# Kernel tuning notes

Measured on AMD Instinct MI355X. Metric: run time of the kernel, lower is better.

The kernel has to match this reference:

```python
import jax, jax.numpy as jnp
import numpy as np
from jax import lax

N_CLASS, SOS, EOS, NEG = 5, 0, 4, -10000.0


def _lstm_dir(x, Wih, Whh, bih, bhh, reverse):
    # x: (T, B, Din); PyTorch gate order i, f, g, o
    T, B, _ = x.shape
    Hd = Whh.shape[1]
    h0 = jnp.zeros((B, Hd), x.dtype)

    def step(carry, xt):
        h, c = carry
        g = xt @ Wih.T + h @ Whh.T + bih + bhh
        i, f, gg, o = jnp.split(g, 4, axis=-1)
        c = jax.nn.sigmoid(f) * c + jax.nn.sigmoid(i) * jnp.tanh(gg)
        h = jax.nn.sigmoid(o) * jnp.tanh(c)
        return (h, c), h

    xs = x[::-1] if reverse else x
    _, hs = lax.scan(step, (h0, h0), xs)
    return hs[::-1] if reverse else hs


def _forward(input_ids, tags, mask, emb, convs, lstm_params, lin_w, lin_b, transition):
    T, B = mask.shape
    x = emb[input_ids][:, None]  # (N, 1, L, E)
    pooled = []
    for w, b in convs:  # w: (K, 1, size, E)
        c = lax.conv_general_dilated(x, w, (1, 1), 'VALID',
                                     dimension_numbers=('NCHW', 'OIHW', 'NCHW'))
        c = jax.nn.relu(c[..., 0] + b[None, :, None])  # (N, K, L-size+1)
        pooled.append(jnp.max(c, axis=2))              # max-pool over length
    para = jnp.concatenate(pooled, axis=1)             # (N, 3K)
    h = para.reshape(B, T, -1).transpose(1, 0, 2)      # (T, B, 3K); equal para_len
    for (Wf, Uf, bf, cf, Wb, Ub, bb, cb) in lstm_params:  # 2-layer BiLSTM (eval: no dropout)
        hf = _lstm_dir(h, Wf, Uf, bf, cf, False)
        hb = _lstm_dir(h, Wb, Ub, bb, cb, True)
        h = jnp.concatenate([hf, hb], axis=-1)
    m = mask[..., None]
    feats = ((h * m) @ lin_w.T + lin_b) * m            # (T, B, 5)

    # CRF forward algorithm (log partition)
    alpha0 = jnp.full((B, N_CLASS), NEG, feats.dtype).at[:, SOS].set(0.0)

    def step(alpha, inp):
        feat, mt = inp
        s = alpha[:, None, :] + transition[None] + feat[:, :, None]
        new = jax.nn.logsumexp(s, axis=-1)
        return new * mt[:, None] + alpha * (1.0 - mt[:, None]), None

    alpha, _ = lax.scan(step, alpha0, (feats, mask))
    fwd_score = jax.nn.logsumexp(alpha + transition[EOS][None], axis=-1)

    # gold path score
    tags_ext = jnp.concatenate([jnp.full((1, B), SOS, tags.dtype), tags], 0)  # (T+1, B)
    emit = jnp.take_along_axis(feats, tags[..., None], axis=-1)[..., 0]       # (T, B)
    trans = transition[tags_ext[1:], tags_ext[:-1]]                           # (T, B)
    gold = jnp.sum((emit + trans) * mask, axis=0)
    lengths = mask.sum(0).astype(jnp.int32)
    last = tags_ext[lengths, jnp.arange(B)]
    gold = gold + transition[EOS, last]
    return (fwd_score - gold).sum()


def setup_inputs() -> dict:
    key = jax.random.key(0)
    ks = jax.random.split(key, 32)
    B, T, L, V, E, K, H = 8, 64, 64, 50000, 768, 256, 64
    N = B * T
    inp = {}
    inp['input_ids'] = jax.random.randint(ks[0], (N, L), 1, V)
    inp['tags'] = jax.random.randint(ks[1], (T, B), 1, 4)  # B/I/O tags
    inp['mask'] = jnp.ones((T, B), jnp.float32)
    inp['para_len'] = jnp.full((B,), T, jnp.int32)
    inp['emb'] = jax.random.normal(ks[2], (V, E)) * 0.1
    for i, sz in enumerate((3, 4, 5)):
        inp[f'cw{sz}'] = jax.random.normal(ks[3 + i], (K, 1, sz, E)) * (1.0 / np.sqrt(sz * E))
        inp[f'cb{sz}'] = jnp.zeros((K,), jnp.float32)
    kidx = 6
    for layer, din in ((0, 3 * K), (1, 2 * H)):
        for d in 'fb':
            inp[f'Wih{layer}{d}'] = jax.random.normal(ks[kidx], (4 * H, din)) * (1.0 / np.sqrt(din)); kidx += 1
            inp[f'Whh{layer}{d}'] = jax.random.normal(ks[kidx], (4 * H, H)) * (1.0 / np.sqrt(H)); kidx += 1
            inp[f'bih{layer}{d}'] = jnp.zeros((4 * H,), jnp.float32)
            inp[f'bhh{layer}{d}'] = jnp.zeros((4 * H,), jnp.float32)
    inp['lin_w'] = jax.random.normal(ks[kidx], (N_CLASS, 2 * H)) * 0.1; kidx += 1
    inp['lin_b'] = jnp.zeros((N_CLASS,), jnp.float32)
    tr = jax.random.normal(ks[kidx], (N_CLASS, N_CLASS))
    inp['transition'] = tr.at[SOS, :].set(NEG).at[:, EOS].set(NEG)
    return inp


def reference(input_ids, tags, mask, para_len, emb, cw3, cb3, cw4, cb4, cw5, cb5,
              Wih0f, Whh0f, bih0f, bhh0f, Wih0b, Whh0b, bih0b, bhh0b,
              Wih1f, Whh1f, bih1f, bhh1f, Wih1b, Whh1b, bih1b, bhh1b,
              lin_w, lin_b, transition):
    convs = ((cw3, cb3), (cw4, cb4), (cw5, cb5))
    lstm_params = ((Wih0f, Whh0f, bih0f, bhh0f, Wih0b, Whh0b, bih0b, bhh0b),
                   (Wih1f, Whh1f, bih1f, bhh1f, Wih1b, Whh1b, bih1b, bhh1b))
    return _forward(input_ids, tags, mask, emb, convs, lstm_params, lin_w, lin_b, transition)
```

## Files before the change

### kernel.cpp

```cpp
#include <hip/hip_runtime.h>
#include <cstdint>
#include <cstddef>

#define DEV __device__ __forceinline__

typedef __bf16 bf16x8 __attribute__((ext_vector_type(8)));
typedef float f32x4 __attribute__((ext_vector_type(4)));

#define NEG_VAL -10000.0f

DEV unsigned int f2bf(float f) {
    unsigned int u = __float_as_uint(f);
    return (u + 0x7FFFu + ((u >> 16) & 1u)) >> 16;
}
DEV unsigned int pk2(float a, float b) { return f2bf(a) | (f2bf(b) << 16); }

DEV float sigf(float x)  { return __builtin_amdgcn_rcpf(1.f + __expf(-x)); }
DEV float tanhff(float x){ return 2.f * __builtin_amdgcn_rcpf(1.f + __expf(-2.f * x)) - 1.f; }

__global__ void cast_all_kernel(const float* __restrict__ cw3,
                                const float* __restrict__ cw4,
                                const float* __restrict__ cw5,
                                const float* __restrict__ Wih0f,
                                const float* __restrict__ Wih0b,
                                const float* __restrict__ Wih1f,
                                const float* __restrict__ Wih1b,
                                unsigned short* __restrict__ wbc,
                                unsigned short* __restrict__ wih0c,
                                unsigned short* __restrict__ wih1c) {
    int tid = blockIdx.x * blockDim.x + threadIdx.x;
    const float* src;
    uint4* dstp;
    if (tid < 294912) {
        int g   = tid & 3;
        int col = (tid >> 2) & 255;
        int c   = (tid >> 10) % 24;
        int p   = tid / (24 * 256 * 4);
        int sz, j; const float* W;
        if (p < 3)      { sz = 3; j = p;     W = cw3; }
        else if (p < 7) { sz = 4; j = p - 3; W = cw4; }
        else            { sz = 5; j = p - 7; W = cw5; }
        src = W + ((size_t)col * sz + j) * 768 + c * 32 + g * 8;
        dstp = reinterpret_cast<uint4*>(wbc) +
               ((size_t)(p * 24 + c) * 1024 + (col >> 4) * 64 + g * 16 + (col & 15));
    } else if (tid < 294912 + 49152) {
        int u   = tid - 294912;
        int g   = u & 3;
        int col = (u >> 2) & 255;
        int kc  = (u >> 10) % 24;
        int dir = u / (24 * 256 * 4);
        const float* W = dir ? Wih0b : Wih0f;
        src = W + (size_t)col * 768 + kc * 32 + g * 8;
        dstp = reinterpret_cast<uint4*>(wih0c) +
               ((size_t)(dir * 24 + kc) * 1024 + (col >> 4) * 64 + g * 16 + (col & 15));
    } else if (tid < 294912 + 49152 + 8192) {
        int u   = tid - 294912 - 49152;
        int g   = u & 3;
        int col = (u >> 2) & 255;
        int kc  = (u >> 10) % 4;
        int dir = u / (4 * 256 * 4);
        const float* W = dir ? Wih1b : Wih1f;
        src = W + (size_t)col * 128 + kc * 32 + g * 8;
        dstp = reinterpret_cast<uint4*>(wih1c) +
               ((size_t)(dir * 4 + kc) * 1024 + (col >> 4) * 64 + g * 16 + (col & 15));
    } else return;
    float4 a = *(const float4*)(src);
    float4 b = *(const float4*)(src + 4);
    *dstp = make_uint4(pk2(a.x, a.y), pk2(a.z, a.w), pk2(b.x, b.y), pk2(b.z, b.w));
}

template<int SZ>
DEV void conv_body(const int* __restrict__ ids,
                   const float* __restrict__ emb,
                   const unsigned short* __restrict__ wbc,
                   const float* __restrict__ cb,
                   unsigned short* __restrict__ para_bf,
                   int pair, int szi, int pbase,
                   unsigned short* Xlds)
{
    int tid  = threadIdx.x;
    int lane = tid & 63;
    int nw   = tid >> 6;
    int l15  = lane & 15;
    int q    = lane >> 4;
    int n0   = pair * 2;

    int srow  = tid >> 1;
    int shalf = tid & 1;
    int sid   = ids[(n0 + (srow >> 6)) * 64 + (srow & 63)];
    const float* embrow = emb + (size_t)sid * 768 + shalf * 16;
    int skey = (srow >> 1) & 3;
    int xo0 = srow * 32 + (((2 * shalf)     ^ skey) * 8);
    int xo1 = srow * 32 + (((2 * shalf + 1) ^ skey) * 8);

    int vlaneB = nw * 2048 + lane * 8;

    f32x4 acc[8][4];
    #pragma unroll
    for (int a = 0; a < 8; a++)
        #pragma unroll
        for (int t = 0; t < 4; t++) acc[a][t] = (f32x4){0.f, 0.f, 0.f, 0.f};

    bf16x8 bfr[2][4];
    float4 e0, e1, e2, e3;

    {
        e0 = ((const float4*)embrow)[0];
        e1 = ((const float4*)embrow)[1];
        e2 = ((const float4*)embrow)[2];
        e3 = ((const float4*)embrow)[3];
        const unsigned short* bt = wbc + (size_t)(pbase * 24) * 8192 + vlaneB;
        #pragma unroll
        for (int t = 0; t < 4; t++)
            bfr[0][t] = *(const bf16x8*)(bt + t * 512);
        uint4 p0 = make_uint4(pk2(e0.x, e0.y), pk2(e0.z, e0.w),
                              pk2(e1.x, e1.y), pk2(e1.z, e1.w));
        uint4 p1 = make_uint4(pk2(e2.x, e2.y), pk2(e2.z, e2.w),
                              pk2(e3.x, e3.y), pk2(e3.z, e3.w));
        *(uint4*)&Xlds[xo0] = p0;
        *(uint4*)&Xlds[xo1] = p1;
        asm volatile("s_waitcnt lgkmcnt(0)" ::: "memory");
        __builtin_amdgcn_s_barrier();
    }

    int cbase = pbase * 24;
    for (int c2 = 0; c2 < 24; c2 += 2, cbase += 2) {
        #pragma unroll
        for (int s2 = 0; s2 < 2 * SZ; ++s2) {
            const int half = (s2 < SZ) ? 0 : 1;
            const int j    = s2 - half * SZ;
            const int par  = s2 & 1;
            {
                const int sP = s2 + 1;
                const int offP = (sP < SZ) ? sP * 24
                               : (sP < 2 * SZ ? (sP - SZ) * 24 + 1 : 2);
                const unsigned short* bt =
                    wbc + (size_t)(cbase + offP) * 8192 + vlaneB;
                #pragma unroll
                for (int t = 0; t < 4; t++)
                    bfr[par ^ 1][t] = *(const bf16x8*)(bt + t * 512);
            }
            if (s2 == 0 || s2 == SZ) {
                int cE = half ? c2 + 2 : c2 + 1; if (cE > 23) cE = 0;
                const float* sp = embrow + cE * 32;
                e0 = ((const float4*)sp)[0];
                e1 = ((const float4*)sp)[1];
                e2 = ((const float4*)sp)[2];
                e3 = ((const float4*)sp)[3];
            }

            const unsigned short* Xb = Xlds + half * 4096;
            {
                bf16x8 af[4];
                #pragma unroll
                for (int a = 0; a < 4; a++) {
                    int pp = 16 * a + l15 + j; if (pp > 63) pp = 63;
                    af[a] = *(const bf16x8*)(
                        &Xb[pp * 32 + ((q ^ ((pp >> 1) & 3)) * 8)]);
                }
                __builtin_amdgcn_s_setprio(1);
                #pragma unroll
                for (int a = 0; a < 4; a++)
                    #pragma unroll
                    for (int t = 0; t < 4; t++)
                        acc[a][t] = __builtin_amdgcn_mfma_f32_16x16x32_bf16(
                            af[a], bfr[par][t], acc[a][t], 0, 0, 0);
                __builtin_amdgcn_s_setprio(0);
            }
            {
                bf16x8 af[4];
                #pragma unroll
                for (int a = 0; a < 4; a++) {
                    int pp = 16 * a + l15 + j; if (pp > 63) pp = 63;
                    int xr = 64 + pp;
                    af[a] = *(const bf16x8*)(
                        &Xb[xr * 32 + ((q ^ ((xr >> 1) & 3)) * 8)]);
                }
                __builtin_amdgcn_s_setprio(1);
                #pragma unroll
                for (int a = 0; a < 4; a++)
                    #pragma unroll
                    for (int t = 0; t < 4; t++)
                        acc[4 + a][t] = __builtin_amdgcn_mfma_f32_16x16x32_bf16(
                            af[a], bfr[par][t], acc[4 + a][t], 0, 0, 0);
                __builtin_amdgcn_s_setprio(0);
            }

            if (j == SZ - 1) {
                unsigned short* Xw = Xlds + (half ^ 1) * 4096;
                uint4 p0 = make_uint4(pk2(e0.x, e0.y), pk2(e0.z, e0.w),
                                      pk2(e1.x, e1.y), pk2(e1.z, e1.w));
                uint4 p1 = make_uint4(pk2(e2.x, e2.y), pk2(e2.z, e2.w),
                                      pk2(e3.x, e3.y), pk2(e3.z, e3.w));
                *(uint4*)&Xw[xo0] = p0;
                *(uint4*)&Xw[xo1] = p1;
                asm volatile("s_waitcnt lgkmcnt(0)" ::: "memory");
                __builtin_amdgcn_s_barrier();
            }
        }
    }

    int pmax = 64 - SZ;
    #pragma unroll
    for (int t = 0; t < 4; t++) {
        int colb = nw * 64 + t * 16;
        float bias = cb[colb + l15];
        #pragma unroll
        for (int s = 0; s < 2; s++) {
            float m = 0.0f;
            #pragma unroll
            for (int a4 = 0; a4 < 4; a4++) {
                #pragma unroll
                for (int r = 0; r < 4; r++) {
                    int p = 16 * a4 + q * 4 + r;
                    float v = acc[s * 4 + a4][t][r] + bias;
                    v = v > 0.f ? v : 0.f;
                    if (p <= pmax) m = v > m ? v : m;
                }
            }
            m = fmaxf(m, __shfl_xor(m, 16));
            m = fmaxf(m, __shfl_xor(m, 32));
            if (lane < 16) {
                int n = n0 + s;
                int row = (n & 63) * 8 + (n >> 6);
                para_bf[(size_t)row * 768 + szi * 256 + colb + lane] =
                    (unsigned short)f2bf(m);
            }
        }
    }
}

__global__ __launch_bounds__(256, 2) void conv_pool_kernel(
    const int* __restrict__ ids,
    const float* __restrict__ emb,
    const unsigned short* __restrict__ wbc,
    const float* __restrict__ cb3, const float* __restrict__ cb4,
    const float* __restrict__ cb5,
    unsigned short* __restrict__ para_bf)
{
    __shared__ unsigned short Xlds[2][4096];
    int bx   = blockIdx.x;
    int szi  = bx >> 8;
    int pair = bx & 255;
    if (szi == 0)
        conv_body<3>(ids, emb, wbc, cb3, para_bf, pair, 0, 0, &Xlds[0][0]);
    else if (szi == 1)
        conv_body<4>(ids, emb, wbc, cb4, para_bf, pair, 1, 3, &Xlds[0][0]);
    else
        conv_body<5>(ids, emb, wbc, cb5, para_bf, pair, 2, 7, &Xlds[0][0]);
}

template<int KC>
__global__ __launch_bounds__(256) void gemm_in_kernel(
    const unsigned short* __restrict__ xbf,
    const unsigned short* __restrict__ wihc,
    const float* __restrict__ bihF, const float* __restrict__ bhhF,
    const float* __restrict__ bihB, const float* __restrict__ bhhB,
    float* __restrict__ gates)
{
    const int din = KC * 32;
    int bx   = blockIdx.x;
    int dir  = bx >> 3;
    int rowg = (bx >> 1) & 3;
    int colg = bx & 1;
    int tid  = threadIdx.x;
    int lane = tid & 63;
    int wid  = tid >> 6;
    int mw   = wid >> 1;
    int nw   = wid & 1;
    int l15  = lane & 15;
    int q    = lane >> 4;

    const float* bih = dir ? bihB : bihF;
    const float* bhh = dir ? bhhB : bhhF;
    const unsigned short* wt = wihc + (size_t)dir * KC * 8192;

    const unsigned short* arow[4];
    #pragma unroll
    for (int a = 0; a < 4; a++)
        arow[a] = xbf + (size_t)(rowg * 128 + mw * 64 + a * 16 + l15) * din + q * 8;
    const unsigned short* bbase = wt + (colg * 8 + nw * 4) * 512 + lane * 8;

    f32x4 acc[4][4];
    #pragma unroll
    for (int a = 0; a < 4; a++)
        #pragma unroll
        for (int t = 0; t < 4; t++) acc[a][t] = (f32x4){0.f, 0.f, 0.f, 0.f};

    bf16x8 afb[2][4], bfb[2][4];
    #pragma unroll
    for (int a = 0; a < 4; a++) afb[0][a] = *(const bf16x8*)(arow[a]);
    #pragma unroll
    for (int t = 0; t < 4; t++) bfb[0][t] = *(const bf16x8*)(bbase + t * 512);

    #pragma unroll 2
    for (int kc = 0; kc < KC; ++kc) {
        const int p = kc & 1;
        int kn = (kc + 1 < KC) ? kc + 1 : kc;
        #pragma unroll
        for (int a = 0; a < 4; a++)
            afb[p ^ 1][a] = *(const bf16x8*)(arow[a] + kn * 32);
        #pragma unroll
        for (int t = 0; t < 4; t++)
            bfb[p ^ 1][t] = *(const bf16x8*)(bbase + (size_t)kn * 8192 + t * 512);
        __builtin_amdgcn_s_setprio(1);
        #pragma unroll
        for (int a = 0; a < 4; a++)
            #pragma unroll
            for (int t = 0; t < 4; t++)
                acc[a][t] = __builtin_amdgcn_mfma_f32_16x16x32_bf16(
                    afb[p][a], bfb[p][t], acc[a][t], 0, 0, 0);
        __builtin_amdgcn_s_setprio(0);
    }

    #pragma unroll
    for (int t = 0; t < 4; t++) {
        int nn = colg * 128 + nw * 64 + t * 16 + l15;
        float bb = bih[nn] + bhh[nn];
        float* gp = gates + ((size_t)dir * 256 + nn) * 512 +
                    rowg * 128 + mw * 64 + q * 4;
        #pragma unroll
        for (int a = 0; a < 4; a++) {
            f32x4 v = acc[a][t];
            v[0] += bb; v[1] += bb; v[2] += bb; v[3] += bb;
            *(f32x4*)(gp + a * 16) = v;
        }
    }
}

__global__ __launch_bounds__(256) void lstm_rec_kernel(
    const float* __restrict__ gates,
    const float* __restrict__ WhhF, const float* __restrict__ WhhB,
    float* __restrict__ houtF,
    unsigned short* __restrict__ houtB)
{
    int dir = blockIdx.x;
    const float* Whh = dir ? WhhB : WhhF;
    const float* gin = gates + (size_t)dir * 256 * 512;

    __shared__ unsigned short h16[2][16 * 64];

    int tid  = threadIdx.x;
    int lane = tid & 63;
    int w    = tid >> 6;
    int l15  = lane & 15;
    int q    = lane >> 4;
    int hh   = 16 * w + l15;

    bf16x8 Bf[4][2];
    #pragma unroll
    for (int g = 0; g < 4; g++)
        #pragma unroll
        for (int kh = 0; kh < 2; kh++) {
            const float* wp = Whh + (size_t)(g * 64 + hh) * 64 + kh * 32 + q * 8;
            float4 f0 = *(const float4*)wp;
            float4 f1 = *(const float4*)(wp + 4);
            bf16x8 r;
            r[0] = (__bf16)f0.x; r[1] = (__bf16)f0.y;
            r[2] = (__bf16)f0.z; r[3] = (__bf16)f0.w;
            r[4] = (__bf16)f1.x; r[5] = (__bf16)f1.y;
            r[6] = (__bf16)f1.z; r[7] = (__bf16)f1.w;
            Bf[g][kh] = r;
        }

    const float* pg0 = gin + ((size_t)(0 * 64 + hh)) * 512 + 4 * (q & 1);
    const float* pg1 = gin + ((size_t)(1 * 64 + hh)) * 512 + 4 * (q & 1);
    const float* pg2 = gin + ((size_t)(2 * 64 + hh)) * 512 + 4 * (q & 1);
    const float* pg3 = gin + ((size_t)(3 * 64 + hh)) * 512 + 4 * (q & 1);

    for (int i = tid; i < 2 * 16 * 64; i += 256)
        ((unsigned short*)h16)[i] = 0;
    float cst[4] = {0.f, 0.f, 0.f, 0.f};
    __syncthreads();

    int t0 = dir ? 63 : 0;
    f32x4 gv0 = *(const f32x4*)(pg0 + t0 * 8);
    f32x4 gv1 = *(const f32x4*)(pg1 + t0 * 8);
    f32x4 gv2 = *(const f32x4*)(pg2 + t0 * 8);
    f32x4 gv3 = *(const f32x4*)(pg3 + t0 * 8);

    for (int s = 0; s < 64; ++s) {
        int t = dir ? 63 - s : s;
        const unsigned short* hb = h16[s & 1];
        int slot0 = q ^ (l15 & 7);
        int slot1 = (4 + q) ^ (l15 & 7);
        bf16x8 a0 = *(const bf16x8*)&hb[l15 * 64 + slot0 * 8];
        bf16x8 a1 = *(const bf16x8*)&hb[l15 * 64 + slot1 * 8];

        f32x4 zero = (f32x4){0.f, 0.f, 0.f, 0.f};
        f32x4 acc[4];
        #pragma unroll
        for (int g = 0; g < 4; g++) {
            acc[g] = __builtin_amdgcn_mfma_f32_16x16x32_bf16(a0, Bf[g][0], zero, 0, 0, 0);
            acc[g] = __builtin_amdgcn_mfma_f32_16x16x32_bf16(a1, Bf[g][1], acc[g], 0, 0, 0);
        }

        int sn = (s + 1 < 64) ? s + 1 : 63;
        int t2 = dir ? 63 - sn : sn;
        f32x4 n0 = *(const f32x4*)(pg0 + t2 * 8);
        f32x4 n1 = *(const f32x4*)(pg1 + t2 * 8);
        f32x4 n2 = *(const f32x4*)(pg2 + t2 * 8);
        f32x4 n3 = *(const f32x4*)(pg3 + t2 * 8);

        if (q < 2) {
            unsigned short* hw = h16[(s + 1) & 1];
            #pragma unroll
            for (int r = 0; r < 4; r++) {
                int b = 4 * q + r;
                float gi = acc[0][r] + gv0[r];
                float gf = acc[1][r] + gv1[r];
                float gg = acc[2][r] + gv2[r];
                float go = acc[3][r] + gv3[r];
                float cn = sigf(gf) * cst[r] + sigf(gi) * tanhff(gg);
                float hv = sigf(go) * tanhff(cn);
                cst[r] = cn;
                int slot = (hh >> 3) ^ (b & 7);
                hw[b * 64 + slot * 8 + (hh & 7)] = (unsigned short)f2bf(hv);
                size_t oi = ((size_t)t * 8 + b) * 128 + dir * 64 + hh;
                if (houtF) houtF[oi] = hv;
                houtB[oi] = (unsigned short)f2bf(hv);
            }
        }
        __syncthreads();
        gv0 = n0; gv1 = n1; gv2 = n2; gv3 = n3;
    }
}

__global__ __launch_bounds__(512) void crf_kernel(
    const float* __restrict__ h1,
    const float* __restrict__ lin_w,
    const float* __restrict__ lin_b,
    const float* __restrict__ mask,
    const int* __restrict__ tags,
    const float* __restrict__ trans,
    float* __restrict__ out) {
    __shared__ float feats[64][8][5];
    __shared__ float wl[5][128];
    __shared__ float msk[512];
    __shared__ int   tgs[512];
    __shared__ float fwd_s[8], gold_s[8];
    __shared__ float tr[25], trE[5], lb[5];
    int tid = threadIdx.x;
    if (tid < 25) tr[tid] = trans[tid];
    if (tid < 5) { trE[tid] = trans[20 + tid]; lb[tid] = lin_b[tid]; }
    msk[tid] = mask[tid];
    tgs[tid] = tags[tid];
    if (tid < 128) {
        #pragma unroll
        for (int i = 0; i < 5; i++) wl[i][tid] = lin_w[i * 128 + tid];
    }
    __syncthreads();

    {
        const float4* h4 = (const float4*)(h1 + (size_t)tid * 128);
        float a0 = 0.f, a1 = 0.f, a2 = 0.f, a3 = 0.f, a4 = 0.f;
        for (int e4 = 0; e4 < 32; e4++) {
            float4 hv = h4[e4];
            int e = e4 * 4;
            a0 += hv.x * wl[0][e] + hv.y * wl[0][e+1] + hv.z * wl[0][e+2] + hv.w * wl[0][e+3];
            a1 += hv.x * wl[1][e] + hv.y * wl[1][e+1] + hv.z * wl[1][e+2] + hv.w * wl[1][e+3];
            a2 += hv.x * wl[2][e] + hv.y * wl[2][e+1] + hv.z * wl[2][e+2] + hv.w * wl[2][e+3];
            a3 += hv.x * wl[3][e] + hv.y * wl[3][e+1] + hv.z * wl[3][e+2] + hv.w * wl[3][e+3];
            a4 += hv.x * wl[4][e] + hv.y * wl[4][e+1] + hv.z * wl[4][e+2] + hv.w * wl[4][e+3];
        }
        float m = msk[tid];
        int t = tid >> 3, b = tid & 7;
        feats[t][b][0] = (m * a0 + lb[0]) * m;
        feats[t][b][1] = (m * a1 + lb[1]) * m;
        feats[t][b][2] = (m * a2 + lb[2]) * m;
        feats[t][b][3] = (m * a3 + lb[3]) * m;
        feats[t][b][4] = (m * a4 + lb[4]) * m;
    }
    __syncthreads();

    if (tid < 40) {
        int b = tid / 5, i = tid % 5;
        float alpha = (i == 0) ? 0.f : NEG_VAL;
        float trow[5];
        #pragma unroll
        for (int j2 = 0; j2 < 5; j2++) trow[j2] = tr[i * 5 + j2];
        for (int t = 0; t < 64; t++) {
            float s0, s1, s2, s3, s4;
            s0 = __shfl(alpha, b * 5 + 0, 64) + trow[0];
            s1 = __shfl(alpha, b * 5 + 1, 64) + trow[1];
            s2 = __shfl(alpha, b * 5 + 2, 64) + trow[2];
            s3 = __shfl(alpha, b * 5 + 3, 64) + trow[3];
            s4 = __shfl(alpha, b * 5 + 4, 64) + trow[4];
            float mx = fmaxf(fmaxf(fmaxf(s0, s1), fmaxf(s2, s3)), s4);
            float sum = expf(s0 - mx) + expf(s1 - mx) + expf(s2 - mx) +
                        expf(s3 - mx) + expf(s4 - mx);
            float lse = mx + logf(sum) + feats[t][b][i];
            float mt = msk[t * 8 + b];
            alpha = mt * lse + (1.f - mt) * alpha;
        }
        float v = alpha + trE[i];
        float m0 = __shfl(v, b * 5 + 0, 64);
        float m1 = __shfl(v, b * 5 + 1, 64);
        float m2 = __shfl(v, b * 5 + 2, 64);
        float m3 = __shfl(v, b * 5 + 3, 64);
        float m4 = __shfl(v, b * 5 + 4, 64);
        float mx = fmaxf(fmaxf(fmaxf(m0, m1), fmaxf(m2, m3)), m4);
        float sum = expf(m0 - mx) + expf(m1 - mx) + expf(m2 - mx) +
                    expf(m3 - mx) + expf(m4 - mx);
        if (i == 0) fwd_s[b] = mx + logf(sum);
    }
    if (tid >= 64 && tid < 72) {
        int b = tid - 64;
        float g = 0.f, lenf = 0.f;
        int prev = 0;
        for (int t = 0; t < 64; t++) {
            int tg = tgs[t * 8 + b];
            float mt = msk[t * 8 + b];
            g += (feats[t][b][tg] + tr[tg * 5 + prev]) * mt;
            lenf += mt;
            prev = tg;
        }
        int len = (int)lenf;
        int last = (len == 0) ? 0 : tgs[(len - 1) * 8 + b];
        g += trE[last];
        gold_s[b] = g;
    }
    __syncthreads();
    if (tid == 0) {
        float s = 0.f;
        for (int b = 0; b < 8; b++) s += fwd_s[b] - gold_s[b];
        out[0] = s;
    }
}

extern "C" void kernel_launch(void* const* d_in, const int* in_sizes, int n_in,
                              void* d_out, int out_size, void* d_ws, size_t ws_size,
                              hipStream_t stream) {
    const int*   ids   = (const int*)d_in[0];
    const int*   tags  = (const int*)d_in[1];
    const float* mask  = (const float*)d_in[2];
    const float* emb   = (const float*)d_in[4];
    const float* cw3   = (const float*)d_in[5];
    const float* cb3   = (const float*)d_in[6];
    const float* cw4   = (const float*)d_in[7];
    const float* cb4   = (const float*)d_in[8];
    const float* cw5   = (const float*)d_in[9];
    const float* cb5   = (const float*)d_in[10];
    const float* Wih0f = (const float*)d_in[11];
    const float* Whh0f = (const float*)d_in[12];
    const float* bih0f = (const float*)d_in[13];
    const float* bhh0f = (const float*)d_in[14];
    const float* Wih0b = (const float*)d_in[15];
    const float* Whh0b = (const float*)d_in[16];
    const float* bih0b = (const float*)d_in[17];
    const float* bhh0b = (const float*)d_in[18];
    const float* Wih1f = (const float*)d_in[19];
    const float* Whh1f = (const float*)d_in[20];
    const float* bih1f = (const float*)d_in[21];
    const float* bhh1f = (const float*)d_in[22];
    const float* Wih1b = (const float*)d_in[23];
    const float* Whh1b = (const float*)d_in[24];
    const float* bih1b = (const float*)d_in[25];
    const float* bhh1b = (const float*)d_in[26];
    const float* lin_w = (const float*)d_in[27];
    const float* lin_b = (const float*)d_in[28];
    const float* trans = (const float*)d_in[29];

    char* ws = (char*)d_ws;
    unsigned short* wbc     = (unsigned short*)ws;
    unsigned short* wih0c   = (unsigned short*)(ws + 4718592);
    unsigned short* wih1c   = (unsigned short*)(ws + 5505024);
    unsigned short* para_bf = (unsigned short*)(ws + 5636096);
    float*          gates   = (float*)(ws + 6422528);
    unsigned short* h0_bf   = (unsigned short*)(ws + 5636096);
    float*          h1f     = (float*)(ws + 4718592);

    hipLaunchKernelGGL(cast_all_kernel, dim3(1376), dim3(256), 0, stream,
                       cw3, cw4, cw5, Wih0f, Wih0b, Wih1f, Wih1b,
                       wbc, wih0c, wih1c);
    hipLaunchKernelGGL(conv_pool_kernel, dim3(768), dim3(256), 0, stream,
                       ids, emb, wbc, cb3, cb4, cb5, para_bf);
    hipLaunchKernelGGL((gemm_in_kernel<24>), dim3(16), dim3(256), 0, stream,
                       para_bf, wih0c, bih0f, bhh0f, bih0b, bhh0b, gates);
    hipLaunchKernelGGL(lstm_rec_kernel, dim3(2), dim3(256), 0, stream,
                       gates, Whh0f, Whh0b, (float*)nullptr, h0_bf);
    hipLaunchKernelGGL((gemm_in_kernel<4>), dim3(16), dim3(256), 0, stream,
                       h0_bf, wih1c, bih1f, bhh1f, bih1b, bhh1b, gates);
    hipLaunchKernelGGL(lstm_rec_kernel, dim3(2), dim3(256), 0, stream,
                       gates, Whh1f, Whh1b, h1f, h0_bf);
    hipLaunchKernelGGL(crf_kernel, dim3(1), dim3(512), 0, stream,
                       h1f, lin_w, lin_b, mask, tags, trans, (float*)d_out);
}
```

Measured before the change: 283.0 us.

## Split input GEMM across more blocks, deepen prefetch, fold gate bias into MFMA

The input-projection GEMM now runs on 32 blocks with half-size row tiles, triple-buffered register prefetch two k-steps ahead, and no setprio hints. The LSTM recurrence seeds the MFMA accumulator with the precomputed input gates instead of adding them afterwards, and loads the gate vector per quad. Conv blocks are also reordered so the largest filter size is scheduled first. The aim is more CU parallelism in a tiny GEMM and fewer ops on the serial recurrence path, at the cost of reloading weights more often and higher register pressure.

```diff
diff --git a/kernel.cpp b/kernel.cpp
--- a/kernel.cpp
+++ b/kernel.cpp
@@ -240,7 +240,7 @@
 {
     __shared__ unsigned short Xlds[2][4096];
     int bx   = blockIdx.x;
-    int szi  = bx >> 8;
+    int szi  = 2 - (bx >> 8);
     int pair = bx & 255;
     if (szi == 0)
         conv_body<3>(ids, emb, wbc, cb3, para_bf, pair, 0, 0, &Xlds[0][0]);
@@ -260,8 +260,8 @@
 {
     const int din = KC * 32;
     int bx   = blockIdx.x;
-    int dir  = bx >> 3;
-    int rowg = (bx >> 1) & 3;
+    int dir  = bx >> 4;
+    int rowg = (bx >> 1) & 7;
     int colg = bx & 1;
     int tid  = threadIdx.x;
     int lane = tid & 63;
@@ -275,42 +275,49 @@
     const float* bhh = dir ? bhhB : bhhF;
     const unsigned short* wt = wihc + (size_t)dir * KC * 8192;
 
-    const unsigned short* arow[4];
-    #pragma unroll
-    for (int a = 0; a < 4; a++)
-        arow[a] = xbf + (size_t)(rowg * 128 + mw * 64 + a * 16 + l15) * din + q * 8;
+    const unsigned short* arow[2];
+    #pragma unroll
+    for (int a = 0; a < 2; a++)
+        arow[a] = xbf + (size_t)(rowg * 64 + mw * 32 + a * 16 + l15) * din + q * 8;
     const unsigned short* bbase = wt + (colg * 8 + nw * 4) * 512 + lane * 8;
 
-    f32x4 acc[4][4];
-    #pragma unroll
-    for (int a = 0; a < 4; a++)
+    f32x4 acc[2][4];
+    #pragma unroll
+    for (int a = 0; a < 2; a++)
         #pragma unroll
         for (int t = 0; t < 4; t++) acc[a][t] = (f32x4){0.f, 0.f, 0.f, 0.f};
 
-    bf16x8 afb[2][4], bfb[2][4];
-    #pragma unroll
-    for (int a = 0; a < 4; a++) afb[0][a] = *(const bf16x8*)(arow[a]);
-    #pragma unroll
-    for (int t = 0; t < 4; t++) bfb[0][t] = *(const bf16x8*)(bbase + t * 512);
-
-    #pragma unroll 2
+    bf16x8 afb[3][2], bfb[3][4];
+    #pragma unroll
+    for (int s = 0; s < 3; s++) {
+        int k0 = (s < KC) ? s : KC - 1;
+        if (s < 2) {
+            #pragma unroll
+            for (int a = 0; a < 2; a++)
+                afb[s][a] = *(const bf16x8*)(arow[a] + k0 * 32);
+            #pragma unroll
+            for (int t = 0; t < 4; t++)
+                bfb[s][t] = *(const bf16x8*)(bbase + (size_t)k0 * 8192 + t * 512);
+        }
+    }
+
+    #pragma unroll 3
     for (int kc = 0; kc < KC; ++kc) {
-        const int p = kc & 1;
-        int kn = (kc + 1 < KC) ? kc + 1 : kc;
-        #pragma unroll
-        for (int a = 0; a < 4; a++)
-            afb[p ^ 1][a] = *(const bf16x8*)(arow[a] + kn * 32);
+        const int p = kc % 3;
+        int kn = (kc + 2 < KC) ? kc + 2 : KC - 1;
+        const int pn = (kc + 2) % 3;
+        #pragma unroll
+        for (int a = 0; a < 2; a++)
+            afb[pn][a] = *(const bf16x8*)(arow[a] + kn * 32);
         #pragma unroll
         for (int t = 0; t < 4; t++)
-            bfb[p ^ 1][t] = *(const bf16x8*)(bbase + (size_t)kn * 8192 + t * 512);
-        __builtin_amdgcn_s_setprio(1);
-        #pragma unroll
-        for (int a = 0; a < 4; a++)
+            bfb[pn][t] = *(const bf16x8*)(bbase + (size_t)kn * 8192 + t * 512);
+        #pragma unroll
+        for (int a = 0; a < 2; a++)
             #pragma unroll
             for (int t = 0; t < 4; t++)
                 acc[a][t] = __builtin_amdgcn_mfma_f32_16x16x32_bf16(
                     afb[p][a], bfb[p][t], acc[a][t], 0, 0, 0);
-        __builtin_amdgcn_s_setprio(0);
     }
 
     #pragma unroll
@@ -318,9 +325,9 @@
         int nn = colg * 128 + nw * 64 + t * 16 + l15;
         float bb = bih[nn] + bhh[nn];
         float* gp = gates + ((size_t)dir * 256 + nn) * 512 +
-                    rowg * 128 + mw * 64 + q * 4;
-        #pragma unroll
-        for (int a = 0; a < 4; a++) {
+                    rowg * 64 + mw * 32 + q * 4;
+        #pragma unroll
+        for (int a = 0; a < 2; a++) {
             f32x4 v = acc[a][t];
             v[0] += bb; v[1] += bb; v[2] += bb; v[3] += bb;
             *(f32x4*)(gp + a * 16) = v;
@@ -363,10 +370,10 @@
             Bf[g][kh] = r;
         }
 
-    const float* pg0 = gin + ((size_t)(0 * 64 + hh)) * 512 + 4 * (q & 1);
-    const float* pg1 = gin + ((size_t)(1 * 64 + hh)) * 512 + 4 * (q & 1);
-    const float* pg2 = gin + ((size_t)(2 * 64 + hh)) * 512 + 4 * (q & 1);
-    const float* pg3 = gin + ((size_t)(3 * 64 + hh)) * 512 + 4 * (q & 1);
+    const float* pg[4];
+    #pragma unroll
+    for (int g = 0; g < 4; g++)
+        pg[g] = gin + ((size_t)(g * 64 + hh)) * 512 + 4 * q;
 
     for (int i = tid; i < 2 * 16 * 64; i += 256)
         ((unsigned short*)h16)[i] = 0;
@@ -374,10 +381,9 @@
     __syncthreads();
 
     int t0 = dir ? 63 : 0;
-    f32x4 gv0 = *(const f32x4*)(pg0 + t0 * 8);
-    f32x4 gv1 = *(const f32x4*)(pg1 + t0 * 8);
-    f32x4 gv2 = *(const f32x4*)(pg2 + t0 * 8);
-    f32x4 gv3 = *(const f32x4*)(pg3 + t0 * 8);
+    f32x4 gv[4];
+    #pragma unroll
+    for (int g = 0; g < 4; g++) gv[g] = *(const f32x4*)(pg[g] + t0 * 8);
 
     for (int s = 0; s < 64; ++s) {
         int t = dir ? 63 - s : s;
@@ -387,30 +393,29 @@
         bf16x8 a0 = *(const bf16x8*)&hb[l15 * 64 + slot0 * 8];
         bf16x8 a1 = *(const bf16x8*)&hb[l15 * 64 + slot1 * 8];
 
-        f32x4 zero = (f32x4){0.f, 0.f, 0.f, 0.f};
         f32x4 acc[4];
         #pragma unroll
         for (int g = 0; g < 4; g++) {
-            acc[g] = __builtin_amdgcn_mfma_f32_16x16x32_bf16(a0, Bf[g][0], zero, 0, 0, 0);
+            acc[g] = __builtin_amdgcn_mfma_f32_16x16x32_bf16(a0, Bf[g][0], gv[g], 0, 0, 0);
             acc[g] = __builtin_amdgcn_mfma_f32_16x16x32_bf16(a1, Bf[g][1], acc[g], 0, 0, 0);
         }
 
         int sn = (s + 1 < 64) ? s + 1 : 63;
         int t2 = dir ? 63 - sn : sn;
-        f32x4 n0 = *(const f32x4*)(pg0 + t2 * 8);
-        f32x4 n1 = *(const f32x4*)(pg1 + t2 * 8);
-        f32x4 n2 = *(const f32x4*)(pg2 + t2 * 8);
-        f32x4 n3 = *(const f32x4*)(pg3 + t2 * 8);
+        f32x4 n0 = *(const f32x4*)(pg[0] + t2 * 8);
+        f32x4 n1 = *(const f32x4*)(pg[1] + t2 * 8);
+        f32x4 n2 = *(const f32x4*)(pg[2] + t2 * 8);
+        f32x4 n3 = *(const f32x4*)(pg[3] + t2 * 8);
 
         if (q < 2) {
             unsigned short* hw = h16[(s + 1) & 1];
             #pragma unroll
             for (int r = 0; r < 4; r++) {
                 int b = 4 * q + r;
-                float gi = acc[0][r] + gv0[r];
-                float gf = acc[1][r] + gv1[r];
-                float gg = acc[2][r] + gv2[r];
-                float go = acc[3][r] + gv3[r];
+                float gi = acc[0][r];
+                float gf = acc[1][r];
+                float gg = acc[2][r];
+                float go = acc[3][r];
                 float cn = sigf(gf) * cst[r] + sigf(gi) * tanhff(gg);
                 float hv = sigf(go) * tanhff(cn);
                 cst[r] = cn;
@@ -422,7 +427,7 @@
             }
         }
         __syncthreads();
-        gv0 = n0; gv1 = n1; gv2 = n2; gv3 = n3;
+        gv[0] = n0; gv[1] = n1; gv[2] = n2; gv[3] = n3;
     }
 }
 
@@ -575,11 +580,11 @@
                        wbc, wih0c, wih1c);
     hipLaunchKernelGGL(conv_pool_kernel, dim3(768), dim3(256), 0, stream,
                        ids, emb, wbc, cb3, cb4, cb5, para_bf);
-    hipLaunchKernelGGL((gemm_in_kernel<24>), dim3(16), dim3(256), 0, stream,
+    hipLaunchKernelGGL((gemm_in_kernel<24>), dim3(32), dim3(256), 0, stream,
                        para_bf, wih0c, bih0f, bhh0f, bih0b, bhh0b, gates);
     hipLaunchKernelGGL(lstm_rec_kernel, dim3(2), dim3(256), 0, stream,
                        gates, Whh0f, Whh0b, (float*)nullptr, h0_bf);
-    hipLaunchKernelGGL((gemm_in_kernel<4>), dim3(16), dim3(256), 0, stream,
+    hipLaunchKernelGGL((gemm_in_kernel<4>), dim3(32), dim3(256), 0, stream,
                        h0_bf, wih1c, bih1f, bhh1f, bih1b, bhh1b, gates);
     hipLaunchKernelGGL(lstm_rec_kernel, dim3(2), dim3(256), 0, stream,
                        gates, Whh1f, Whh1b, h1f, h0_bf);
```

Measured after the change: 275.3 us. 2.7% less time.
